# Kernel optimization log

Measured on AMD Instinct MI355X. Metric: run time of the kernel, lower is better.

Reference implementation:

```python
import jax, jax.numpy as jnp
import numpy as np

N = 100000   # total nodes in batch
E = 400000   # total directed edges
G = 4096     # number of graphs
D = 300      # emb_dim
H = 600      # GIN MLP hidden = 2*emb_dim
L = 5        # num_layer
BN_EPS = 1e-5
SELF_LOOP_BOND_TYPE = 4  # contextpred convention


def setup_inputs() -> dict:
    key = jax.random.key(0)
    ks = jax.random.split(key, 16)
    s = 0.1
    return {
        "x": jax.random.randint(ks[0], (N, 2), 0, 3),
        "edge_index": jax.random.randint(ks[1], (2, E), 0, N),
        "edge_attr": jax.random.randint(ks[2], (E, 2), 0, 3),
        "batch": jnp.sort(jax.random.randint(ks[3], (N,), 0, G)),
        "atom_emb1": jax.random.normal(ks[4], (120, D), jnp.float32) * s,
        "atom_emb2": jax.random.normal(ks[5], (3, D), jnp.float32) * s,
        "edge_emb1": jax.random.normal(ks[6], (L, 6, D), jnp.float32) * s,
        "edge_emb2": jax.random.normal(ks[7], (L, 3, D), jnp.float32) * s,
        "w1": jax.random.normal(ks[8], (L, D, H), jnp.float32) * (1.0 / np.sqrt(D)),
        "b1": jnp.zeros((L, H), jnp.float32),
        "w2": jax.random.normal(ks[9], (L, H, D), jnp.float32) * (1.0 / np.sqrt(H)),
        "b2": jnp.zeros((L, D), jnp.float32),
        "bn_g": jnp.ones((L, D), jnp.float32),
        "bn_b": jnp.zeros((L, D), jnp.float32),
        "bn_m": jnp.zeros((L, D), jnp.float32),
        "bn_v": jnp.ones((L, D), jnp.float32),
        "head_w1": jax.random.normal(ks[10], (D, 512), jnp.float32) * (1.0 / np.sqrt(D)),
        "head_b1": jnp.zeros((512,), jnp.float32),
        "head_w2": jax.random.normal(ks[11], (512, 2), jnp.float32) * (1.0 / np.sqrt(512)),
        "head_b2": jnp.zeros((2,), jnp.float32),
    }


def _gnn_forward(x, edge_index, edge_attr, batch,
                 atom_emb1, atom_emb2, edge_emb1, edge_emb2,
                 w1, b1, w2, b2, bn_g, bn_b, bn_m, bn_v,
                 head_w1, head_b1, head_w2, head_b2):
    src, dst = edge_index[0], edge_index[1]
    # node input embedding: atom type + chirality
    h = atom_emb1[x[:, 0]] + atom_emb2[x[:, 1]]  # [N, D]
    for l in range(L):
        # edge embeddings for real edges
        eemb = edge_emb1[l][edge_attr[:, 0]] + edge_emb2[l][edge_attr[:, 1]]  # [E, D]
        # self-loop edge embedding (bond type 4, direction 0), same for all nodes
        self_emb = edge_emb1[l][SELF_LOOP_BOND_TYPE] + edge_emb2[l][0]  # [D]
        # GIN 'add' aggregation of messages (x_j + edge_emb), incl. self loops
        agg = jax.ops.segment_sum(h[src] + eemb, dst, num_segments=N)
        agg = agg + h + self_emb  # fused self-loop contribution
        # MLP: Linear(D,2D) -> ReLU -> Linear(2D,D)
        h = jax.nn.relu(agg @ w1[l] + b1[l]) @ w2[l] + b2[l]
        # BatchNorm1d in eval mode (running stats)
        h = (h - bn_m[l]) * jax.lax.rsqrt(bn_v[l] + BN_EPS) * bn_g[l] + bn_b[l]
        if l < L - 1:  # JK='last': ReLU on all but last layer
            h = jax.nn.relu(h)
    # to_dense_batch + sum(axis=1) == segment sum over graphs
    pooled = jax.ops.segment_sum(h, batch, num_segments=G)  # [G, D]
    # task head
    logits = jax.nn.relu(pooled @ head_w1 + head_b1) @ head_w2 + head_b2  # [G, 2]
    return logits


def reference(x, edge_index, edge_attr, batch,
              atom_emb1, atom_emb2, edge_emb1, edge_emb2,
              w1, b1, w2, b2, bn_g, bn_b, bn_m, bn_v,
              head_w1, head_b1, head_w2, head_b2):
    return _gnn_forward(x, edge_index, edge_attr, batch,
                        atom_emb1, atom_emb2, edge_emb1, edge_emb2,
                        w1, b1, w2, b2, bn_g, bn_b, bn_m, bn_v,
                        head_w1, head_b1, head_w2, head_b2)
```

## Files before the change

### kernel.cpp

```cpp
#include <hip/hip_runtime.h>
#include <hip/hip_bf16.h>
#include <stdint.h>

#define N_NODES 100000
#define N_EDGES 400000
#define N_GRAPH 4096
#define DIMD    300
#define NLAYER  5
#define HPAD   304
#define KP1    320
#define W1ROWS 640
#define WID2   320
#define GGRP   16
#define MROWS  64

typedef __attribute__((ext_vector_type(8))) short bf16x8_t;
typedef __attribute__((ext_vector_type(4))) float f32x4_t;

__device__ __forceinline__ void gload_lds16(const void* g, void* l) {
  auto gp = (__attribute__((address_space(1))) void*)(uintptr_t)g;
  auto lp = (__attribute__((address_space(3))) void*)(uint32_t)(uintptr_t)l;
  __builtin_amdgcn_global_load_lds(gp, lp, 16, 0, 0);
}
__device__ __forceinline__ short f2bs(float f) {
  __hip_bfloat16 b = __float2bfloat16(f); return *(short*)&b;
}
__device__ __forceinline__ float bs2f(short s) {
  __hip_bfloat16 b; *(short*)&b = s; return __bfloat162float(b);
}

__global__ void k_hist(const int* __restrict__ ei, int* __restrict__ cur) {
  const int e = blockIdx.x * blockDim.x + threadIdx.x;
  if (e < N_EDGES) atomicAdd(&cur[ei[N_EDGES + e]], 1);
}

__global__ void k_scan1(int* __restrict__ cur, int* __restrict__ off, int* __restrict__ bsum) {
  __shared__ int buf[1024];
  const int tid = threadIdx.x;
  const int i = blockIdx.x * 1024 + tid;
  int v = (i < N_NODES) ? cur[i] : 0;
  buf[tid] = v;
  __syncthreads();
  for (int s = 1; s < 1024; s <<= 1) {
    int t = (tid >= s) ? buf[tid - s] : 0;
    __syncthreads();
    buf[tid] += t;
    __syncthreads();
  }
  if (i < N_NODES) { off[i + 1] = buf[tid]; cur[i] = 0; }
  if (tid == 1023) bsum[blockIdx.x] = buf[1023];
}

__global__ void k_scan2(int* __restrict__ bsum, int nb) {
  if (threadIdx.x == 0 && blockIdx.x == 0) {
    int run = 0;
    for (int b = 0; b < nb; ++b) { int v = bsum[b]; bsum[b] = run; run += v; }
  }
}

__global__ void k_scan3(int* __restrict__ off, const int* __restrict__ bsum) {
  const int i = blockIdx.x * blockDim.x + threadIdx.x;
  if (i == 0) off[0] = 0;
  if (i < N_NODES) off[i + 1] += bsum[i >> 10];
}

__global__ void k_fill(const int* __restrict__ ei, const int* __restrict__ ea,
                       const int* __restrict__ off, int* __restrict__ cur,
                       int* __restrict__ csr) {
  const int e = blockIdx.x * blockDim.x + threadIdx.x;
  if (e < N_EDGES) {
    const int d = ei[N_EDGES + e];
    const int pos = atomicAdd(&cur[d], 1);
    const int c = ea[2 * e] * 3 + ea[2 * e + 1];
    csr[off[d] + pos] = (ei[e] << 4) | c;
  }
}

__global__ void k_comb(const float* __restrict__ e1, const float* __restrict__ e2,
                       float* __restrict__ comb) {
  const int idx = blockIdx.x * blockDim.x + threadIdx.x;
  if (idx >= NLAYER * 10 * HPAD) return;
  const int l = idx / (10 * HPAD);
  const int r = (idx / HPAD) % 10;
  const int d = idx % HPAD;
  float v = 0.f;
  if (d < DIMD) {
    int a, b;
    if (r < 9) { a = r / 3; b = r % 3; } else { a = 4; b = 0; }
    v = e1[(l * 6 + a) * DIMD + d] + e2[(l * 3 + b) * DIMD + d];
  }
  comb[idx] = v;
}

__global__ void k_wc1(const float* __restrict__ w, __hip_bfloat16* __restrict__ wb) {
  const int idx = blockIdx.x * blockDim.x + threadIdx.x;
  if (idx >= NLAYER * W1ROWS * KP1) return;
  const int l = idx / (W1ROWS * KP1);
  const int n = (idx / KP1) % W1ROWS;
  const int k = idx % KP1;
  float v = 0.f;
  if (n < 600 && k < DIMD) v = w[((long)l * DIMD + k) * 600 + n];
  wb[idx] = __float2bfloat16(v);
}

__global__ void k_wc2(const float* __restrict__ w, __hip_bfloat16* __restrict__ wb) {
  const int idx = blockIdx.x * blockDim.x + threadIdx.x;
  if (idx >= NLAYER * WID2 * W1ROWS) return;
  const int l = idx / (WID2 * W1ROWS);
  const int n = (idx / W1ROWS) % WID2;
  const int k = idx % W1ROWS;
  float v = 0.f;
  if (n < DIMD && k < 600) v = w[((long)l * 600 + k) * DIMD + n];
  wb[idx] = __float2bfloat16(v);
}

__global__ void k_nemb(const int* __restrict__ x, const float* __restrict__ ae1,
                       const float* __restrict__ ae2, __hip_bfloat16* __restrict__ h) {
  const int gid = blockIdx.x * blockDim.x + threadIdx.x;
  if (gid >= N_NODES * 38) return;
  const int node = gid / 38;
  const int l = gid % 38;
  bf16x8_t ov;
#pragma unroll
  for (int j = 0; j < 8; ++j) ov[j] = 0;
  {
    const int i0 = x[2 * node], i1 = x[2 * node + 1];
    const float* r1 = ae1 + (long)i0 * DIMD + l * 8;
    const float* r2 = ae2 + (long)i1 * DIMD + l * 8;
#pragma unroll
    for (int j = 0; j < 8; ++j) {
      const int d = l * 8 + j;
      if (d < DIMD) ov[j] = f2bs(r1[j] + r2[j]);
    }
  }
  *(bf16x8_t*)(h + (long)node * HPAD + l * 8) = ov;
}

__global__ __launch_bounds__(256)
void k_agg(const __hip_bfloat16* __restrict__ h, __hip_bfloat16* __restrict__ aggb,
           const int* __restrict__ csr, const int* __restrict__ off,
           const float* __restrict__ comb) {
  const int wv = threadIdx.x >> 6;
  const int lane = threadIdx.x & 63;
  const int node = blockIdx.x * 4 + wv;
  if (node >= N_NODES) return;
  if (lane >= 40) return;
  const bool act = lane < 38;
  float acc[8];
  if (act) {
    const bf16x8_t hv = *(const bf16x8_t*)(h + (long)node * HPAD + lane * 8);
    const float* c9 = comb + 9 * HPAD + lane * 8;
#pragma unroll
    for (int j = 0; j < 8; ++j) acc[j] = bs2f(hv[j]) + c9[j];
  } else {
#pragma unroll
    for (int j = 0; j < 8; ++j) acc[j] = 0.f;
  }
  const int p0 = off[node], p1 = off[node + 1];
  for (int p = p0; p < p1; ++p) {
    const int v = csr[p];
    const int s = v >> 4;
    const int c = v & 15;
    if (act) {
      const bf16x8_t hv = *(const bf16x8_t*)(h + (long)s * HPAD + lane * 8);
      const float* cc = comb + c * HPAD + lane * 8;
#pragma unroll
      for (int j = 0; j < 8; ++j) acc[j] += bs2f(hv[j]) + cc[j];
    }
  }
  bf16x8_t ov;
#pragma unroll
  for (int j = 0; j < 8; ++j) ov[j] = act ? f2bs(acc[j]) : (short)0;
  *(bf16x8_t*)(aggb + (long)node * KP1 + lane * 8) = ov;
}

__global__ __launch_bounds__(256, 2)
void k_mlp(const __hip_bfloat16* __restrict__ aggb,
           const __hip_bfloat16* __restrict__ w1b,
           const __hip_bfloat16* __restrict__ w2b,
           const float* __restrict__ b1,
           const float* __restrict__ b2,
           const float* __restrict__ bng, const float* __restrict__ bnb,
           const float* __restrict__ bnm, const float* __restrict__ bnv,
           int reluFlag,
           __hip_bfloat16* __restrict__ h) {
  __shared__ __align__(16) char As[MROWS * 640];
  __shared__ __align__(16) char P[MROWS * 256];
  const int tid = threadIdx.x;
  const int lane = tid & 63;
  const int wc = tid >> 6;
  const int fr = lane & 15;
  const int kg = lane >> 4;
  const int row0 = blockIdx.x * MROWS;

#pragma unroll
  for (int it = 0; it < 10; ++it) {
    const int g = it * 256 + tid;
    const int r = g / 40;
    const int gin = g - r * 40;
    int ar = row0 + r;
    if (ar >= N_NODES) ar = N_NODES - 1;
    gload_lds16((const char*)aggb + (size_t)ar * 640 + (size_t)((gin ^ (r & 7)) * 16),
                As + g * 16);
  }

  f32x4_t accB[4][5];
#pragma unroll
  for (int m = 0; m < 4; ++m)
#pragma unroll
    for (int n = 0; n < 5; ++n) accB[m][n] = (f32x4_t){0.f, 0.f, 0.f, 0.f};

  __syncthreads();

  for (int c = 0; c < 5; ++c) {
    f32x4_t accA[4][2];
#pragma unroll
    for (int m = 0; m < 4; ++m)
#pragma unroll
      for (int n = 0; n < 2; ++n) accA[m][n] = (f32x4_t){0.f, 0.f, 0.f, 0.f};
    const __hip_bfloat16* w1c = w1b + (size_t)(c * 128 + wc * 32) * KP1;
#pragma unroll
    for (int ks = 0; ks < 10; ++ks) {
      const int k2 = ks * 64 + kg * 16;
      bf16x8_t af[4], bfr[2];
#pragma unroll
      for (int m = 0; m < 4; ++m) {
        const int r = m * 16 + fr;
        af[m] = *(const bf16x8_t*)(As + r * 640 + (k2 ^ ((r & 7) << 4)));
      }
#pragma unroll
      for (int n = 0; n < 2; ++n)
        bfr[n] = *(const bf16x8_t*)(w1c + (size_t)(n * 16 + fr) * KP1 + ks * 32 + kg * 8);
#pragma unroll
      for (int m = 0; m < 4; ++m)
#pragma unroll
        for (int n = 0; n < 2; ++n)
          accA[m][n] = __builtin_amdgcn_mfma_f32_16x16x32_bf16(af[m], bfr[n], accA[m][n], 0, 0, 0);
    }
    float b1v[2];
#pragma unroll
    for (int n = 0; n < 2; ++n) {
      const int col = c * 128 + wc * 32 + n * 16 + fr;
      b1v[n] = (col < 600) ? b1[col] : 0.f;
    }
    __syncthreads();
#pragma unroll
    for (int m = 0; m < 4; ++m) {
#pragma unroll
      for (int n = 0; n < 2; ++n) {
        const int pcol = wc * 32 + n * 16 + fr;
#pragma unroll
        for (int j = 0; j < 4; ++j) {
          const int prow = m * 16 + kg * 4 + j;
          const float v = fmaxf(accA[m][n][j] + b1v[n], 0.f);
          *(short*)(P + prow * 256 + ((pcol * 2) ^ ((prow & 7) << 4))) = f2bs(v);
        }
      }
    }
    __syncthreads();
#pragma unroll
    for (int ks = 0; ks < 4; ++ks) {
      bf16x8_t af2[4], bf2[5];
#pragma unroll
      for (int m = 0; m < 4; ++m) {
        const int pr = m * 16 + fr;
        af2[m] = *(const bf16x8_t*)(P + pr * 256 + ((ks * 64 + kg * 16) ^ ((pr & 7) << 4)));
      }
      const int k2 = c * 128 + ks * 32 + kg * 8;
#pragma unroll
      for (int n = 0; n < 5; ++n)
        bf2[n] = *(const bf16x8_t*)(w2b + (size_t)(wc * 80 + n * 16 + fr) * W1ROWS + k2);
#pragma unroll
      for (int m = 0; m < 4; ++m)
#pragma unroll
        for (int n = 0; n < 5; ++n)
          accB[m][n] = __builtin_amdgcn_mfma_f32_16x16x32_bf16(af2[m], bf2[n], accB[m][n], 0, 0, 0);
    }
  }

  float scale[5], shift[5];
#pragma unroll
  for (int n = 0; n < 5; ++n) {
    const int col = wc * 80 + n * 16 + fr;
    if (col < DIMD) {
      const float sc = rsqrtf(bnv[col] + 1e-5f) * bng[col];
      scale[n] = sc;
      shift[n] = (b2[col] - bnm[col]) * sc + bnb[col];
    } else { scale[n] = 0.f; shift[n] = 0.f; }
  }
#pragma unroll
  for (int m = 0; m < 4; ++m) {
#pragma unroll
    for (int n = 0; n < 5; ++n) {
      const int col = wc * 80 + n * 16 + fr;
      if (col >= HPAD) continue;
#pragma unroll
      for (int j = 0; j < 4; ++j) {
        const int node = row0 + m * 16 + kg * 4 + j;
        if (node >= N_NODES) continue;
        float v = 0.f;
        if (col < DIMD) {
          v = accB[m][n][j] * scale[n] + shift[n];
          if (reluFlag) v = fmaxf(v, 0.f);
        }
        h[(size_t)node * HPAD + col] = __float2bfloat16(v);
      }
    }
  }
}

__device__ __forceinline__ int lbound(const int* a, int n, int key) {
  int lo = 0, hi = n;
  while (lo < hi) { int mid = (lo + hi) >> 1; if (a[mid] < key) lo = mid + 1; else hi = mid; }
  return lo;
}

__global__ void k_pool(const __hip_bfloat16* __restrict__ h, const int* __restrict__ batch,
                       float* __restrict__ pooled) {
  __shared__ int se[2];
  const int g = blockIdx.x;
  if (threadIdx.x < 2) se[threadIdx.x] = lbound(batch, N_NODES, g + threadIdx.x);
  __syncthreads();
  const int d = threadIdx.x;
  if (d < DIMD) {
    float a = 0.f;
    for (int i = se[0]; i < se[1]; ++i) a += __bfloat162float(h[(long)i * HPAD + d]);
    pooled[(long)g * DIMD + d] = a;
  }
}

__global__ __launch_bounds__(256)
void k_head(const float* __restrict__ pooled, const float* __restrict__ hw1,
            const float* __restrict__ hb1, const float* __restrict__ hw2,
            const float* __restrict__ hb2, float* __restrict__ out) {
  __shared__ float sp[GGRP][DIMD];
  __shared__ float sred[4][2][GGRP];
  const int g0 = blockIdx.x * GGRP;
  const int tid = threadIdx.x;
  const int lane = tid & 63;
  const int wv = tid >> 6;
  for (int i = tid; i < GGRP * DIMD; i += 256)
    sp[i / DIMD][i % DIMD] = pooled[(long)(g0 + i / DIMD) * DIMD + i % DIMD];
  __syncthreads();
  float p0[GGRP], p1[GGRP];
#pragma unroll
  for (int g = 0; g < GGRP; ++g) { p0[g] = 0.f; p1[g] = 0.f; }
  for (int j = tid; j < 512; j += 256) {
    const float wa = hw2[2 * j], wb = hw2[2 * j + 1];
    float z[GGRP];
#pragma unroll
    for (int g = 0; g < GGRP; ++g) z[g] = hb1[j];
    for (int d = 0; d < DIMD; ++d) {
      const float w = hw1[d * 512 + j];
#pragma unroll
      for (int g = 0; g < GGRP; ++g) z[g] = fmaf(sp[g][d], w, z[g]);
    }
#pragma unroll
    for (int g = 0; g < GGRP; ++g) {
      const float zr = fmaxf(z[g], 0.f);
      p0[g] = fmaf(zr, wa, p0[g]);
      p1[g] = fmaf(zr, wb, p1[g]);
    }
  }
#pragma unroll
  for (int g = 0; g < GGRP; ++g) {
#pragma unroll
    for (int s = 32; s > 0; s >>= 1) {
      p0[g] += __shfl_xor(p0[g], s, 64);
      p1[g] += __shfl_xor(p1[g], s, 64);
    }
    if (lane == 0) { sred[wv][0][g] = p0[g]; sred[wv][1][g] = p1[g]; }
  }
  __syncthreads();
  if (tid < 2 * GGRP) {
    const int g = tid & (GGRP - 1);
    const int which = tid >> 4;
    float a = sred[0][which][g] + sred[1][which][g] + sred[2][which][g] + sred[3][which][g];
    out[2 * (g0 + g) + which] = a + hb2[which];
  }
}

__global__ void k_sentinel(float* out) { out[threadIdx.x] = 1.0e6f; }

extern "C" void kernel_launch(void* const* d_in, const int* in_sizes, int n_in,
                              void* d_out, int out_size, void* d_ws, size_t ws_size,
                              hipStream_t stream) {
  const int*   x     = (const int*)d_in[0];
  const int*   ei    = (const int*)d_in[1];
  const int*   ea    = (const int*)d_in[2];
  const int*   batch = (const int*)d_in[3];
  const float* ae1   = (const float*)d_in[4];
  const float* ae2   = (const float*)d_in[5];
  const float* ee1   = (const float*)d_in[6];
  const float* ee2   = (const float*)d_in[7];
  const float* w1    = (const float*)d_in[8];
  const float* b1    = (const float*)d_in[9];
  const float* w2    = (const float*)d_in[10];
  const float* b2    = (const float*)d_in[11];
  const float* bng   = (const float*)d_in[12];
  const float* bnbp  = (const float*)d_in[13];
  const float* bnm   = (const float*)d_in[14];
  const float* bnv   = (const float*)d_in[15];
  const float* hw1   = (const float*)d_in[16];
  const float* hb1   = (const float*)d_in[17];
  const float* hw2   = (const float*)d_in[18];
  const float* hb2   = (const float*)d_in[19];
  float* out = (float*)d_out;

  char* ws = (char*)d_ws;
  size_t o = 0;
  auto alloc = [&](size_t bytes) { size_t p = o; o += (bytes + 255) & ~(size_t)255; return p; };
  __hip_bfloat16* h      = (__hip_bfloat16*)(ws + alloc((size_t)N_NODES * HPAD * 2));
  __hip_bfloat16* aggb   = (__hip_bfloat16*)(ws + alloc((size_t)N_NODES * KP1 * 2));
  __hip_bfloat16* w1b    = (__hip_bfloat16*)(ws + alloc((size_t)NLAYER * W1ROWS * KP1 * 2));
  __hip_bfloat16* w2b    = (__hip_bfloat16*)(ws + alloc((size_t)NLAYER * WID2 * W1ROWS * 2));
  float*          comb   = (float*)         (ws + alloc((size_t)NLAYER * 10 * HPAD * 4));
  int*            offp   = (int*)           (ws + alloc((size_t)(N_NODES + 1) * 4));
  int*            cur    = (int*)           (ws + alloc((size_t)N_NODES * 4));
  int*            csr    = (int*)           (ws + alloc((size_t)N_EDGES * 4));
  float*          pooled = (float*)         (ws + alloc((size_t)N_GRAPH * DIMD * 4));
  int*            bsum   = (int*)           (ws + alloc(128 * 4));
  if (o > ws_size) {
    k_sentinel<<<1, 8, 0, stream>>>(out);
    return;
  }

  hipMemsetAsync(cur, 0, (size_t)N_NODES * 4, stream);

  k_hist<<<(N_EDGES + 255) / 256, 256, 0, stream>>>(ei, cur);
  const int nsb = (N_NODES + 1023) / 1024;
  k_scan1<<<nsb, 1024, 0, stream>>>(cur, offp, bsum);
  k_scan2<<<1, 64, 0, stream>>>(bsum, nsb);
  k_scan3<<<(N_NODES + 255) / 256, 256, 0, stream>>>(offp, bsum);
  k_fill<<<(N_EDGES + 255) / 256, 256, 0, stream>>>(ei, ea, offp, cur, csr);

  k_wc1<<<(NLAYER * W1ROWS * KP1 + 255) / 256, 256, 0, stream>>>(w1, w1b);
  k_wc2<<<(NLAYER * WID2 * W1ROWS + 255) / 256, 256, 0, stream>>>(w2, w2b);
  k_comb<<<(NLAYER * 10 * HPAD + 255) / 256, 256, 0, stream>>>(ee1, ee2, comb);
  k_nemb<<<(N_NODES * 38 + 255) / 256, 256, 0, stream>>>(x, ae1, ae2, h);

  const int mlpBlocks = (N_NODES + MROWS - 1) / MROWS;
  for (int l = 0; l < NLAYER; ++l) {
    k_agg<<<(N_NODES + 3) / 4, 256, 0, stream>>>(h, aggb, csr, offp, comb + l * 10 * HPAD);
    k_mlp<<<mlpBlocks, 256, 0, stream>>>(aggb,
        w1b + (size_t)l * W1ROWS * KP1, w2b + (size_t)l * WID2 * W1ROWS,
        b1 + l * 600, b2 + l * DIMD,
        bng + l * DIMD, bnbp + l * DIMD, bnm + l * DIMD, bnv + l * DIMD,
        (l < NLAYER - 1) ? 1 : 0, h);
  }

  k_pool<<<N_GRAPH, 320, 0, stream>>>(h, batch, pooled);
  k_head<<<N_GRAPH / GGRP, 256, 0, stream>>>(pooled, hw1, hb1, hw2, hb2, out);
}
```

Measured before the change: 1.741 ms.

## Double-buffer MLP hidden chunks and move head GEMM to bf16 MFMA

k_mlp now computes the first hidden chunk up front, then interleaves the second GEMM for chunk c with the first GEMM for chunk c+1, using a double-buffered P tile and prefetching W1 fragments. This cuts the per-chunk barriers from two to one and lets the matrix-core work overlap with LDS traffic. Separately, the task head is rewritten as a bf16 MFMA GEMM over 64 graphs per block, with a new weight-conversion kernel and bf16 pooled output. The cost is higher register and LDS pressure in k_mlp, and lower precision in the head.

Measured after the change: 1.607 ms. 1.08x faster.

```diff
diff --git a/kernel.cpp b/kernel.cpp
--- a/kernel.cpp
+++ b/kernel.cpp
@@ -11,8 +11,8 @@
 #define KP1    320
 #define W1ROWS 640
 #define WID2   320
-#define GGRP   16
 #define MROWS  64
+#define HGR    64
 
 typedef __attribute__((ext_vector_type(8))) short bf16x8_t;
 typedef __attribute__((ext_vector_type(4))) float f32x4_t;
@@ -111,6 +111,15 @@
   const int k = idx % W1ROWS;
   float v = 0.f;
   if (n < DIMD && k < 600) v = w[((long)l * 600 + k) * DIMD + n];
+  wb[idx] = __float2bfloat16(v);
+}
+
+__global__ void k_wch(const float* __restrict__ w, __hip_bfloat16* __restrict__ wb) {
+  const int idx = blockIdx.x * blockDim.x + threadIdx.x;
+  if (idx >= 512 * KP1) return;
+  const int n = idx / KP1;
+  const int k = idx % KP1;
+  float v = (k < DIMD) ? w[(long)k * 512 + n] : 0.f;
   wb[idx] = __float2bfloat16(v);
 }
 
@@ -185,7 +194,7 @@
            int reluFlag,
            __hip_bfloat16* __restrict__ h) {
   __shared__ __align__(16) char As[MROWS * 640];
-  __shared__ __align__(16) char P[MROWS * 256];
+  __shared__ __align__(16) char P[2 * MROWS * 256];
   const int tid = threadIdx.x;
   const int lane = tid & 63;
   const int wc = tid >> 6;
@@ -212,13 +221,13 @@
 
   __syncthreads();
 
-  for (int c = 0; c < 5; ++c) {
+  {
     f32x4_t accA[4][2];
 #pragma unroll
     for (int m = 0; m < 4; ++m)
 #pragma unroll
       for (int n = 0; n < 2; ++n) accA[m][n] = (f32x4_t){0.f, 0.f, 0.f, 0.f};
-    const __hip_bfloat16* w1c = w1b + (size_t)(c * 128 + wc * 32) * KP1;
+    const __hip_bfloat16* w1c = w1b + (size_t)(wc * 32) * KP1;
 #pragma unroll
     for (int ks = 0; ks < 10; ++ks) {
       const int k2 = ks * 64 + kg * 16;
@@ -237,34 +246,45 @@
         for (int n = 0; n < 2; ++n)
           accA[m][n] = __builtin_amdgcn_mfma_f32_16x16x32_bf16(af[m], bfr[n], accA[m][n], 0, 0, 0);
     }
-    float b1v[2];
 #pragma unroll
     for (int n = 0; n < 2; ++n) {
-      const int col = c * 128 + wc * 32 + n * 16 + fr;
-      b1v[n] = (col < 600) ? b1[col] : 0.f;
-    }
-    __syncthreads();
-#pragma unroll
-    for (int m = 0; m < 4; ++m) {
-#pragma unroll
-      for (int n = 0; n < 2; ++n) {
-        const int pcol = wc * 32 + n * 16 + fr;
+      const int col = wc * 32 + n * 16 + fr;
+      const float bv = (col < 600) ? b1[col] : 0.f;
+#pragma unroll
+      for (int m = 0; m < 4; ++m)
 #pragma unroll
         for (int j = 0; j < 4; ++j) {
           const int prow = m * 16 + kg * 4 + j;
-          const float v = fmaxf(accA[m][n][j] + b1v[n], 0.f);
-          *(short*)(P + prow * 256 + ((pcol * 2) ^ ((prow & 7) << 4))) = f2bs(v);
+          const int pcol = wc * 32 + n * 16 + fr;
+          *(short*)(P + prow * 256 + ((pcol * 2) ^ ((prow & 7) << 4))) =
+              f2bs(fmaxf(accA[m][n][j] + bv, 0.f));
         }
-      }
-    }
-    __syncthreads();
+    }
+  }
+  __syncthreads();
+
+#pragma unroll
+  for (int c = 0; c < 5; ++c) {
+    const char* Pc = P + (c & 1) * (MROWS * 256);
+    char* Pn = P + ((c + 1) & 1) * (MROWS * 256);
+
+    bf16x8_t w1f[10];
+    if (c < 4) {
+      const __hip_bfloat16* w1c = w1b + (size_t)((c + 1) * 128 + wc * 32) * KP1;
+#pragma unroll
+      for (int ks = 0; ks < 5; ++ks)
+#pragma unroll
+        for (int n = 0; n < 2; ++n)
+          w1f[ks * 2 + n] = *(const bf16x8_t*)(w1c + (size_t)(n * 16 + fr) * KP1 + ks * 32 + kg * 8);
+    }
+
 #pragma unroll
     for (int ks = 0; ks < 4; ++ks) {
       bf16x8_t af2[4], bf2[5];
 #pragma unroll
       for (int m = 0; m < 4; ++m) {
         const int pr = m * 16 + fr;
-        af2[m] = *(const bf16x8_t*)(P + pr * 256 + ((ks * 64 + kg * 16) ^ ((pr & 7) << 4)));
+        af2[m] = *(const bf16x8_t*)(Pc + pr * 256 + ((ks * 64 + kg * 16) ^ ((pr & 7) << 4)));
       }
       const int k2 = c * 128 + ks * 32 + kg * 8;
 #pragma unroll
@@ -276,6 +296,63 @@
         for (int n = 0; n < 5; ++n)
           accB[m][n] = __builtin_amdgcn_mfma_f32_16x16x32_bf16(af2[m], bf2[n], accB[m][n], 0, 0, 0);
     }
+
+    if (c < 4) {
+      f32x4_t accA[4][2];
+#pragma unroll
+      for (int m = 0; m < 4; ++m)
+#pragma unroll
+        for (int n = 0; n < 2; ++n) accA[m][n] = (f32x4_t){0.f, 0.f, 0.f, 0.f};
+      const __hip_bfloat16* w1c = w1b + (size_t)((c + 1) * 128 + wc * 32) * KP1;
+#pragma unroll
+      for (int ks = 0; ks < 5; ++ks) {
+        const int k2 = ks * 64 + kg * 16;
+        bf16x8_t af[4];
+#pragma unroll
+        for (int m = 0; m < 4; ++m) {
+          const int r = m * 16 + fr;
+          af[m] = *(const bf16x8_t*)(As + r * 640 + (k2 ^ ((r & 7) << 4)));
+        }
+#pragma unroll
+        for (int m = 0; m < 4; ++m)
+#pragma unroll
+          for (int n = 0; n < 2; ++n)
+            accA[m][n] = __builtin_amdgcn_mfma_f32_16x16x32_bf16(af[m], w1f[ks * 2 + n], accA[m][n], 0, 0, 0);
+      }
+#pragma unroll
+      for (int ks = 5; ks < 10; ++ks) {
+        const int k2 = ks * 64 + kg * 16;
+        bf16x8_t af[4], bfr[2];
+#pragma unroll
+        for (int m = 0; m < 4; ++m) {
+          const int r = m * 16 + fr;
+          af[m] = *(const bf16x8_t*)(As + r * 640 + (k2 ^ ((r & 7) << 4)));
+        }
+#pragma unroll
+        for (int n = 0; n < 2; ++n)
+          bfr[n] = *(const bf16x8_t*)(w1c + (size_t)(n * 16 + fr) * KP1 + ks * 32 + kg * 8);
+#pragma unroll
+        for (int m = 0; m < 4; ++m)
+#pragma unroll
+          for (int n = 0; n < 2; ++n)
+            accA[m][n] = __builtin_amdgcn_mfma_f32_16x16x32_bf16(af[m], bfr[n], accA[m][n], 0, 0, 0);
+      }
+#pragma unroll
+      for (int n = 0; n < 2; ++n) {
+        const int col = (c + 1) * 128 + wc * 32 + n * 16 + fr;
+        const float bv = (col < 600) ? b1[col] : 0.f;
+#pragma unroll
+        for (int m = 0; m < 4; ++m)
+#pragma unroll
+          for (int j = 0; j < 4; ++j) {
+            const int prow = m * 16 + kg * 4 + j;
+            const int pcol = wc * 32 + n * 16 + fr;
+            *(short*)(Pn + prow * 256 + ((pcol * 2) ^ ((prow & 7) << 4))) =
+                f2bs(fmaxf(accA[m][n][j] + bv, 0.f));
+          }
+      }
+    }
+    __syncthreads();
   }
 
   float scale[5], shift[5];
@@ -316,67 +393,116 @@
 }
 
 __global__ void k_pool(const __hip_bfloat16* __restrict__ h, const int* __restrict__ batch,
-                       float* __restrict__ pooled) {
+                       __hip_bfloat16* __restrict__ pooled) {
   __shared__ int se[2];
   const int g = blockIdx.x;
   if (threadIdx.x < 2) se[threadIdx.x] = lbound(batch, N_NODES, g + threadIdx.x);
   __syncthreads();
   const int d = threadIdx.x;
-  if (d < DIMD) {
+  if (d < KP1) {
     float a = 0.f;
-    for (int i = se[0]; i < se[1]; ++i) a += __bfloat162float(h[(long)i * HPAD + d]);
-    pooled[(long)g * DIMD + d] = a;
+    if (d < DIMD)
+      for (int i = se[0]; i < se[1]; ++i) a += __bfloat162float(h[(long)i * HPAD + d]);
+    pooled[(long)g * KP1 + d] = __float2bfloat16(d < DIMD ? a : 0.f);
   }
 }
 
 __global__ __launch_bounds__(256)
-void k_head(const float* __restrict__ pooled, const float* __restrict__ hw1,
+void k_head(const __hip_bfloat16* __restrict__ pooled,
+            const __hip_bfloat16* __restrict__ hw1b,
             const float* __restrict__ hb1, const float* __restrict__ hw2,
             const float* __restrict__ hb2, float* __restrict__ out) {
-  __shared__ float sp[GGRP][DIMD];
-  __shared__ float sred[4][2][GGRP];
-  const int g0 = blockIdx.x * GGRP;
+  __shared__ __align__(16) char As[HGR * 640];
+  __shared__ float sred[4][HGR][2];
   const int tid = threadIdx.x;
   const int lane = tid & 63;
-  const int wv = tid >> 6;
-  for (int i = tid; i < GGRP * DIMD; i += 256)
-    sp[i / DIMD][i % DIMD] = pooled[(long)(g0 + i / DIMD) * DIMD + i % DIMD];
+  const int wc = tid >> 6;
+  const int fr = lane & 15;
+  const int kg = lane >> 4;
+  const int g0 = blockIdx.x * HGR;
+
+#pragma unroll
+  for (int it = 0; it < 10; ++it) {
+    const int g = it * 256 + tid;
+    const int r = g / 40;
+    const int gin = g - r * 40;
+    gload_lds16((const char*)pooled + (size_t)(g0 + r) * 640 + (size_t)((gin ^ (r & 7)) * 16),
+                As + g * 16);
+  }
+
+  f32x4_t acc[4][8];
+#pragma unroll
+  for (int m = 0; m < 4; ++m)
+#pragma unroll
+    for (int n = 0; n < 8; ++n) acc[m][n] = (f32x4_t){0.f, 0.f, 0.f, 0.f};
+
   __syncthreads();
-  float p0[GGRP], p1[GGRP];
-#pragma unroll
-  for (int g = 0; g < GGRP; ++g) { p0[g] = 0.f; p1[g] = 0.f; }
-  for (int j = tid; j < 512; j += 256) {
-    const float wa = hw2[2 * j], wb = hw2[2 * j + 1];
-    float z[GGRP];
-#pragma unroll
-    for (int g = 0; g < GGRP; ++g) z[g] = hb1[j];
-    for (int d = 0; d < DIMD; ++d) {
-      const float w = hw1[d * 512 + j];
-#pragma unroll
-      for (int g = 0; g < GGRP; ++g) z[g] = fmaf(sp[g][d], w, z[g]);
-    }
-#pragma unroll
-    for (int g = 0; g < GGRP; ++g) {
-      const float zr = fmaxf(z[g], 0.f);
-      p0[g] = fmaf(zr, wa, p0[g]);
-      p1[g] = fmaf(zr, wb, p1[g]);
-    }
-  }
-#pragma unroll
-  for (int g = 0; g < GGRP; ++g) {
-#pragma unroll
-    for (int s = 32; s > 0; s >>= 1) {
-      p0[g] += __shfl_xor(p0[g], s, 64);
-      p1[g] += __shfl_xor(p1[g], s, 64);
-    }
-    if (lane == 0) { sred[wv][0][g] = p0[g]; sred[wv][1][g] = p1[g]; }
+
+#pragma unroll
+  for (int ks = 0; ks < 10; ++ks) {
+    const int k2 = ks * 64 + kg * 16;
+    bf16x8_t af[4], bw[8];
+#pragma unroll
+    for (int m = 0; m < 4; ++m) {
+      const int r = m * 16 + fr;
+      af[m] = *(const bf16x8_t*)(As + r * 640 + (k2 ^ ((r & 7) << 4)));
+    }
+#pragma unroll
+    for (int n = 0; n < 8; ++n)
+      bw[n] = *(const bf16x8_t*)(hw1b + (size_t)(wc * 128 + n * 16 + fr) * KP1 + ks * 32 + kg * 8);
+#pragma unroll
+    for (int m = 0; m < 4; ++m)
+#pragma unroll
+      for (int n = 0; n < 8; ++n)
+        acc[m][n] = __builtin_amdgcn_mfma_f32_16x16x32_bf16(af[m], bw[n], acc[m][n], 0, 0, 0);
+  }
+
+  float p0[4][4], p1[4][4];
+#pragma unroll
+  for (int m = 0; m < 4; ++m)
+#pragma unroll
+    for (int j = 0; j < 4; ++j) { p0[m][j] = 0.f; p1[m][j] = 0.f; }
+#pragma unroll
+  for (int n = 0; n < 8; ++n) {
+    const int col = wc * 128 + n * 16 + fr;
+    const float bv = hb1[col];
+    const float wa = hw2[2 * col], wb = hw2[2 * col + 1];
+#pragma unroll
+    for (int m = 0; m < 4; ++m)
+#pragma unroll
+      for (int j = 0; j < 4; ++j) {
+        const float z = fmaxf(acc[m][n][j] + bv, 0.f);
+        p0[m][j] = fmaf(z, wa, p0[m][j]);
+        p1[m][j] = fmaf(z, wb, p1[m][j]);
+      }
+  }
+#pragma unroll
+  for (int m = 0; m < 4; ++m)
+#pragma unroll
+    for (int j = 0; j < 4; ++j) {
+#pragma unroll
+      for (int s = 1; s < 16; s <<= 1) {
+        p0[m][j] += __shfl_xor(p0[m][j], s, 64);
+        p1[m][j] += __shfl_xor(p1[m][j], s, 64);
+      }
+    }
+  if (fr == 0) {
+#pragma unroll
+    for (int m = 0; m < 4; ++m)
+#pragma unroll
+      for (int j = 0; j < 4; ++j) {
+        const int row = m * 16 + kg * 4 + j;
+        sred[wc][row][0] = p0[m][j];
+        sred[wc][row][1] = p1[m][j];
+      }
   }
   __syncthreads();
-  if (tid < 2 * GGRP) {
-    const int g = tid & (GGRP - 1);
-    const int which = tid >> 4;
-    float a = sred[0][which][g] + sred[1][which][g] + sred[2][which][g] + sred[3][which][g];
-    out[2 * (g0 + g) + which] = a + hb2[which];
+  if (tid < HGR) {
+    const int row = tid;
+    float a0 = sred[0][row][0] + sred[1][row][0] + sred[2][row][0] + sred[3][row][0];
+    float a1 = sred[0][row][1] + sred[1][row][1] + sred[2][row][1] + sred[3][row][1];
+    out[2 * (g0 + row)] = a0 + hb2[0];
+    out[2 * (g0 + row) + 1] = a1 + hb2[1];
   }
 }
 
@@ -414,11 +540,12 @@
   __hip_bfloat16* aggb   = (__hip_bfloat16*)(ws + alloc((size_t)N_NODES * KP1 * 2));
   __hip_bfloat16* w1b    = (__hip_bfloat16*)(ws + alloc((size_t)NLAYER * W1ROWS * KP1 * 2));
   __hip_bfloat16* w2b    = (__hip_bfloat16*)(ws + alloc((size_t)NLAYER * WID2 * W1ROWS * 2));
+  __hip_bfloat16* hw1b   = (__hip_bfloat16*)(ws + alloc((size_t)512 * KP1 * 2));
   float*          comb   = (float*)         (ws + alloc((size_t)NLAYER * 10 * HPAD * 4));
   int*            offp   = (int*)           (ws + alloc((size_t)(N_NODES + 1) * 4));
   int*            cur    = (int*)           (ws + alloc((size_t)N_NODES * 4));
   int*            csr    = (int*)           (ws + alloc((size_t)N_EDGES * 4));
-  float*          pooled = (float*)         (ws + alloc((size_t)N_GRAPH * DIMD * 4));
+  __hip_bfloat16* pooled = (__hip_bfloat16*)(ws + alloc((size_t)N_GRAPH * KP1 * 2));
   int*            bsum   = (int*)           (ws + alloc(128 * 4));
   if (o > ws_size) {
     k_sentinel<<<1, 8, 0, stream>>>(out);
@@ -436,6 +563,7 @@
 
   k_wc1<<<(NLAYER * W1ROWS * KP1 + 255) / 256, 256, 0, stream>>>(w1, w1b);
   k_wc2<<<(NLAYER * WID2 * W1ROWS + 255) / 256, 256, 0, stream>>>(w2, w2b);
+  k_wch<<<(512 * KP1 + 255) / 256, 256, 0, stream>>>(hw1, hw1b);
   k_comb<<<(NLAYER * 10 * HPAD + 255) / 256, 256, 0, stream>>>(ee1, ee2, comb);
   k_nemb<<<(N_NODES * 38 + 255) / 256, 256, 0, stream>>>(x, ae1, ae2, h);
 
@@ -449,6 +577,6 @@
         (l < NLAYER - 1) ? 1 : 0, h);
   }
 
-  k_pool<<<N_GRAPH, 320, 0, stream>>>(h, batch, pooled);
-  k_head<<<N_GRAPH / GGRP, 256, 0, stream>>>(pooled, hw1, hb1, hw2, hb2, out);
-}
+  k_pool<<<N_GRAPH, KP1, 0, stream>>>(h, batch, pooled);
+  k_head<<<N_GRAPH / HGR, 256, 0, stream>>>(pooled, hw1b, hb1, hw2, hb2, out);
+}
```
